# Kernel tuning notes

Hardware: AMD Instinct MI355X
Metric: run time of the kernel (lower is better)

The kernel has to match this reference:

```python
import jax, jax.numpy as jnp
import numpy as np

E = 1024
H = 16
DH = E // H  # projection_dim = 64


def setup_inputs() -> dict:
    key = jax.random.key(0)
    ks = jax.random.split(key, 6)
    B, S = 2, 2048
    s = 1.0 / np.sqrt(E)
    return {
        "features": jax.random.normal(ks[0], (B, S, E), jnp.float32),
        "mask": jnp.zeros((B, 1, 1, S), jnp.float32),
        "Wq": jax.random.normal(ks[1], (E, E), jnp.float32) * s,
        "bq": jnp.zeros((E,), jnp.float32),
        "Wk": jax.random.normal(ks[2], (E, E), jnp.float32) * s,
        "bk": jnp.zeros((E,), jnp.float32),
        "Wv": jax.random.normal(ks[3], (E, E), jnp.float32) * s,
        "bv": jnp.zeros((E,), jnp.float32),
        "Wo": jax.random.normal(ks[4], (E, E), jnp.float32) * s,
        "bo": jnp.zeros((E,), jnp.float32),
    }


def _split_heads(x, B):
    # [B,S,E] -> [B,H,S,DH]
    return x.reshape(B, -1, H, DH).transpose(0, 2, 1, 3)


def reference(features, mask, Wq, bq, Wk, bk, Wv, bv, Wo, bo):
    B, S, _ = features.shape
    q = _split_heads(features @ Wq + bq, B)  # [B,H,S,DH]
    k = _split_heads(features @ Wk + bk, B)
    v = _split_heads(features @ Wv + bv, B)
    logits = jnp.einsum("bhqd,bhkd->bhqk", q, k) / jnp.sqrt(jnp.float32(DH))
    logits = logits + mask * (-1e9)
    attn = jax.nn.softmax(logits, axis=-1)  # [B,H,S,S]
    ctx = jnp.einsum("bhqk,bhkd->bhqd", attn, v)
    ctx = ctx.transpose(0, 2, 1, 3).reshape(B, S, E)
    out = ctx @ Wo + bo
    return out, attn
```

## Files before the change

### kernel.cpp

```cpp
#include <hip/hip_runtime.h>
#include <hip/hip_bf16.h>

typedef __attribute__((ext_vector_type(8))) short bf16x8;
typedef __attribute__((ext_vector_type(4))) float f32x4;

#define B_ 2
#define S_ 2048
#define E_ 1024
#define H_ 16
#define DH_ 64

__global__ __launch_bounds__(256) void cast_bf16_kernel(const float* __restrict__ x,
                                                        __hip_bfloat16* __restrict__ y) {
  int i = blockIdx.x * 256 + threadIdx.x;
  float4 v = reinterpret_cast<const float4*>(x)[i];
  __hip_bfloat16 t[4] = {__float2bfloat16(v.x), __float2bfloat16(v.y),
                         __float2bfloat16(v.z), __float2bfloat16(v.w)};
  reinterpret_cast<uint2*>(y)[i] = *reinterpret_cast<uint2*>(t);
}

__global__ __launch_bounds__(256) void transpose_cast_kernel(const float* __restrict__ W,
                                                             __hip_bfloat16* __restrict__ Wt) {
  __shared__ float t[32][33];
  int bx = blockIdx.x * 32, by = blockIdx.y * 32;
  int tx = threadIdx.x & 31, ty = threadIdx.x >> 5;
  for (int r = 0; r < 32; r += 8)
    t[ty + r][tx] = W[(size_t)(by + ty + r) * E_ + bx + tx];
  __syncthreads();
  for (int r = 0; r < 32; r += 8)
    Wt[(size_t)(bx + ty + r) * E_ + by + tx] = __float2bfloat16(t[tx][ty + r]);
}

#define GT 64
#define GBK 32
__global__ __launch_bounds__(256) void gemm_bt_kernel(
    const __hip_bfloat16* __restrict__ A,
    const __hip_bfloat16* __restrict__ Bt,
    const float* __restrict__ bias_m,
    const float* __restrict__ bias_n,
    __hip_bfloat16* __restrict__ Cb,
    float* __restrict__ Cf,
    int M, int N, int K) {
  __shared__ __hip_bfloat16 As[GT][GBK + 8];
  __shared__ __hip_bfloat16 Bs[GT][GBK + 8];
  const int tid = threadIdx.x;
  const int lane = tid & 63;
  const int wave = tid >> 6;
  const int l15 = lane & 15, l4 = lane >> 4;
  const int m0 = blockIdx.y * GT;
  const int n0 = blockIdx.x * GT;
  const int wm = (wave & 1) * 32;
  const int wn = (wave >> 1) * 32;
  const int srow = tid >> 2;
  const int schunk = (tid & 3) * 8;
  f32x4 acc[2][2] = {};
  for (int k0 = 0; k0 < K; k0 += GBK) {
    __syncthreads();
    *reinterpret_cast<bf16x8*>(&As[srow][schunk]) =
        *reinterpret_cast<const bf16x8*>(&A[(size_t)(m0 + srow) * K + k0 + schunk]);
    *reinterpret_cast<bf16x8*>(&Bs[srow][schunk]) =
        *reinterpret_cast<const bf16x8*>(&Bt[(size_t)(n0 + srow) * K + k0 + schunk]);
    __syncthreads();
    bf16x8 af[2], bfr[2];
#pragma unroll
    for (int i = 0; i < 2; ++i)
      af[i] = *reinterpret_cast<const bf16x8*>(&As[wm + i * 16 + l15][l4 * 8]);
#pragma unroll
    for (int j = 0; j < 2; ++j)
      bfr[j] = *reinterpret_cast<const bf16x8*>(&Bs[wn + j * 16 + l15][l4 * 8]);
#pragma unroll
    for (int i = 0; i < 2; ++i)
#pragma unroll
      for (int j = 0; j < 2; ++j)
        acc[i][j] = __builtin_amdgcn_mfma_f32_16x16x32_bf16(af[i], bfr[j], acc[i][j], 0, 0, 0);
  }
#pragma unroll
  for (int i = 0; i < 2; ++i)
#pragma unroll
    for (int j = 0; j < 2; ++j)
#pragma unroll
      for (int r = 0; r < 4; ++r) {
        int row = m0 + wm + i * 16 + l4 * 4 + r;
        int col = n0 + wn + j * 16 + l15;
        float v = acc[i][j][r];
        if (bias_m) v += bias_m[row];
        if (bias_n) v += bias_n[col];
        if (Cf) Cf[(size_t)row * N + col] = v;
        else    Cb[(size_t)row * N + col] = __float2bfloat16(v);
      }
}

#define QBLK 64
#define KBLK 128
__global__ __launch_bounds__(256) void attn_kernel(
    const __hip_bfloat16* __restrict__ Qb,
    const __hip_bfloat16* __restrict__ Kb,
    const __hip_bfloat16* __restrict__ Vtb,
    const float* __restrict__ mask,
    float* __restrict__ attn_out,
    __hip_bfloat16* __restrict__ Ctxb) {
  __shared__ __hip_bfloat16 Qs[QBLK][DH_ + 8];
  __shared__ __hip_bfloat16 Ks[KBLK][DH_ + 8];
  __shared__ __hip_bfloat16 Vs[DH_][KBLK + 8];
  __shared__ __hip_bfloat16 Ps[QBLK][KBLK + 8];
  const int tid = threadIdx.x;
  const int lane = tid & 63;
  const int wave = tid >> 6;
  const int l15 = lane & 15, l4 = lane >> 4;
  const int bh = blockIdx.y;
  const int b = bh >> 4;
  const int h = bh & 15;
  const int q0 = blockIdx.x * QBLK;

  {
    int row = tid >> 3, c = (tid & 7) * 8;
#pragma unroll
    for (int p = 0; p < 2; ++p) {
      int r = row + p * 32;
      *reinterpret_cast<bf16x8*>(&Qs[r][c]) =
          *reinterpret_cast<const bf16x8*>(&Qb[(size_t)(b * S_ + q0 + r) * E_ + h * DH_ + c]);
    }
  }
  __syncthreads();
  bf16x8 qa0 = *reinterpret_cast<const bf16x8*>(&Qs[wave * 16 + l15][l4 * 8]);
  bf16x8 qa1 = *reinterpret_cast<const bf16x8*>(&Qs[wave * 16 + l15][32 + l4 * 8]);

  float mrow[4], srow[4];
#pragma unroll
  for (int r = 0; r < 4; ++r) { mrow[r] = -1e30f; srow[r] = 0.f; }

  for (int kt = 0; kt < S_ / KBLK; ++kt) {
    __syncthreads();
    { int row = tid >> 3, c = (tid & 7) * 8;
#pragma unroll
      for (int p = 0; p < 4; ++p) {
        int r = row + p * 32;
        *reinterpret_cast<bf16x8*>(&Ks[r][c]) =
            *reinterpret_cast<const bf16x8*>(&Kb[(size_t)(b * S_ + kt * KBLK + r) * E_ + h * DH_ + c]);
      }
    }
    __syncthreads();
    f32x4 sv[8];
#pragma unroll
    for (int j = 0; j < 8; ++j) {
      bf16x8 kb0 = *reinterpret_cast<const bf16x8*>(&Ks[j * 16 + l15][l4 * 8]);
      bf16x8 kb1 = *reinterpret_cast<const bf16x8*>(&Ks[j * 16 + l15][32 + l4 * 8]);
      f32x4 a = {};
      a = __builtin_amdgcn_mfma_f32_16x16x32_bf16(qa0, kb0, a, 0, 0, 0);
      a = __builtin_amdgcn_mfma_f32_16x16x32_bf16(qa1, kb1, a, 0, 0, 0);
      float mv = mask[b * S_ + kt * KBLK + j * 16 + l15] * -1e9f;
#pragma unroll
      for (int r = 0; r < 4; ++r) sv[j][r] = a[r] * 0.125f + mv;
    }
#pragma unroll
    for (int r = 0; r < 4; ++r) {
      float tmax = sv[0][r];
#pragma unroll
      for (int j = 1; j < 8; ++j) tmax = fmaxf(tmax, sv[j][r]);
      for (int m = 1; m < 16; m <<= 1) tmax = fmaxf(tmax, __shfl_xor(tmax, m, 64));
      float newm = fmaxf(mrow[r], tmax);
      float ls = 0.f;
#pragma unroll
      for (int j = 0; j < 8; ++j) ls += __expf(sv[j][r] - newm);
      for (int m = 1; m < 16; m <<= 1) ls += __shfl_xor(ls, m, 64);
      srow[r] = srow[r] * __expf(mrow[r] - newm) + ls;
      mrow[r] = newm;
    }
  }
  float inv_s[4];
#pragma unroll
  for (int r = 0; r < 4; ++r) inv_s[r] = 1.0f / srow[r];

  f32x4 ctx[4] = {};
  float* attn_base = attn_out + (size_t)bh * S_ * S_;
  for (int kt = 0; kt < S_ / KBLK; ++kt) {
    __syncthreads();
    { int row = tid >> 3, c = (tid & 7) * 8;
#pragma unroll
      for (int p = 0; p < 4; ++p) {
        int r = row + p * 32;
        *reinterpret_cast<bf16x8*>(&Ks[r][c]) =
            *reinterpret_cast<const bf16x8*>(&Kb[(size_t)(b * S_ + kt * KBLK + r) * E_ + h * DH_ + c]);
      }
    }
    { int d = tid >> 4, c = (tid & 15) * 8;
#pragma unroll
      for (int p = 0; p < 4; ++p) {
        int dd = d + p * 16;
        *reinterpret_cast<bf16x8*>(&Vs[dd][c]) =
            *reinterpret_cast<const bf16x8*>(&Vtb[(size_t)(h * DH_ + dd) * (B_ * S_) + b * S_ + kt * KBLK + c]);
      }
    }
    __syncthreads();
#pragma unroll
    for (int j = 0; j < 8; ++j) {
      bf16x8 kb0 = *reinterpret_cast<const bf16x8*>(&Ks[j * 16 + l15][l4 * 8]);
      bf16x8 kb1 = *reinterpret_cast<const bf16x8*>(&Ks[j * 16 + l15][32 + l4 * 8]);
      f32x4 a = {};
      a = __builtin_amdgcn_mfma_f32_16x16x32_bf16(qa0, kb0, a, 0, 0, 0);
      a = __builtin_amdgcn_mfma_f32_16x16x32_bf16(qa1, kb1, a, 0, 0, 0);
      float mv = mask[b * S_ + kt * KBLK + j * 16 + l15] * -1e9f;
#pragma unroll
      for (int r = 0; r < 4; ++r) {
        float p = __expf(a[r] * 0.125f + mv - mrow[r]) * inv_s[r];
        int row = wave * 16 + l4 * 4 + r;
        int col = j * 16 + l15;
        attn_base[(size_t)(q0 + row) * S_ + kt * KBLK + col] = p;
        Ps[row][col] = __float2bfloat16(p);
      }
    }
    __syncthreads();
#pragma unroll
    for (int kk = 0; kk < 4; ++kk) {
      bf16x8 pa = *reinterpret_cast<const bf16x8*>(&Ps[wave * 16 + l15][kk * 32 + l4 * 8]);
#pragma unroll
      for (int j2 = 0; j2 < 4; ++j2) {
        bf16x8 vb = *reinterpret_cast<const bf16x8*>(&Vs[j2 * 16 + l15][kk * 32 + l4 * 8]);
        ctx[j2] = __builtin_amdgcn_mfma_f32_16x16x32_bf16(pa, vb, ctx[j2], 0, 0, 0);
      }
    }
  }
#pragma unroll
  for (int j2 = 0; j2 < 4; ++j2)
#pragma unroll
    for (int r = 0; r < 4; ++r) {
      int row = wave * 16 + l4 * 4 + r;
      int col = j2 * 16 + l15;
      Ctxb[(size_t)(b * S_ + q0 + row) * E_ + h * DH_ + col] = __float2bfloat16(ctx[j2][r]);
    }
}

extern "C" void kernel_launch(void* const* d_in, const int* in_sizes, int n_in,
                              void* d_out, int out_size, void* d_ws, size_t ws_size,
                              hipStream_t stream) {
  const float* features = (const float*)d_in[0];
  const float* mask     = (const float*)d_in[1];
  const float* Wq       = (const float*)d_in[2];
  const float* bq       = (const float*)d_in[3];
  const float* Wk       = (const float*)d_in[4];
  const float* bk       = (const float*)d_in[5];
  const float* Wv       = (const float*)d_in[6];
  const float* bv       = (const float*)d_in[7];
  const float* Wo       = (const float*)d_in[8];
  const float* bo       = (const float*)d_in[9];
  float* out  = (float*)d_out;
  float* attn = out + (size_t)B_ * S_ * E_;

  char* ws = (char*)d_ws;
  __hip_bfloat16* Xbf  = (__hip_bfloat16*)(ws);
  __hip_bfloat16* WqT  = (__hip_bfloat16*)(ws + (8ull  << 20));
  __hip_bfloat16* WkT  = (__hip_bfloat16*)(ws + (10ull << 20));
  __hip_bfloat16* WvT  = (__hip_bfloat16*)(ws + (12ull << 20));
  __hip_bfloat16* WoT  = (__hip_bfloat16*)(ws + (14ull << 20));
  __hip_bfloat16* Qb   = (__hip_bfloat16*)(ws + (16ull << 20));
  __hip_bfloat16* Kb   = (__hip_bfloat16*)(ws + (24ull << 20));
  __hip_bfloat16* Vtb  = (__hip_bfloat16*)(ws + (32ull << 20));
  __hip_bfloat16* Ctxb = (__hip_bfloat16*)(ws + (40ull << 20));

  cast_bf16_kernel<<<(B_ * S_ * E_ / 4) / 256, 256, 0, stream>>>(features, Xbf);
  dim3 tg(E_ / 32, E_ / 32);
  transpose_cast_kernel<<<tg, 256, 0, stream>>>(Wq, WqT);
  transpose_cast_kernel<<<tg, 256, 0, stream>>>(Wk, WkT);
  transpose_cast_kernel<<<tg, 256, 0, stream>>>(Wv, WvT);
  transpose_cast_kernel<<<tg, 256, 0, stream>>>(Wo, WoT);

  gemm_bt_kernel<<<dim3(E_ / GT, B_ * S_ / GT), 256, 0, stream>>>(
      Xbf, WqT, nullptr, bq, Qb, nullptr, B_ * S_, E_, E_);
  gemm_bt_kernel<<<dim3(E_ / GT, B_ * S_ / GT), 256, 0, stream>>>(
      Xbf, WkT, nullptr, bk, Kb, nullptr, B_ * S_, E_, E_);
  gemm_bt_kernel<<<dim3(B_ * S_ / GT, E_ / GT), 256, 0, stream>>>(
      WvT, Xbf, bv, nullptr, Vtb, nullptr, E_, B_ * S_, E_);

  attn_kernel<<<dim3(S_ / QBLK, B_ * H_), 256, 0, stream>>>(Qb, Kb, Vtb, mask, attn, Ctxb);

  gemm_bt_kernel<<<dim3(E_ / GT, B_ * S_ / GT), 256, 0, stream>>>(
      Ctxb, WoT, nullptr, bo, nullptr, out, B_ * S_, E_, E_);
}
```

Measured before the change: 817.2 us.

## Enlarge GEMM tiles with direct LDS loads and drop shared staging in attention

The GEMM moves from 64x64 to 128x128 tiles with 4x4 MFMA accumulators per wave and loads global data straight into LDS through global_load_lds, which raises arithmetic intensity and cuts the register round trip. The attention kernel stops staging Q/K/V in shared memory and reads MFMA fragments directly from global memory. It keeps only a per-wave P buffer, so the block-wide barriers go away. The 64MB attention-probability output is now written with nontemporal stores to bypass cache pollution. The risks are fewer GEMM blocks (256 per launch) on a large CU count, uncoalesced global fragment reads for K and V, and an LDS layout without padding that may cause bank conflicts.

```diff
diff --git a/kernel.cpp b/kernel.cpp
--- a/kernel.cpp
+++ b/kernel.cpp
@@ -31,9 +31,16 @@
     Wt[(size_t)(bx + ty + r) * E_ + by + tx] = __float2bfloat16(t[tx][ty + r]);
 }
 
-#define GT 64
-#define GBK 32
-__global__ __launch_bounds__(256) void gemm_bt_kernel(
+__device__ __forceinline__ void load16_to_lds(const __hip_bfloat16* g, __hip_bfloat16* l) {
+  __builtin_amdgcn_global_load_lds(
+      (const __attribute__((address_space(1))) void*)g,
+      (__attribute__((address_space(3))) void*)l, 16, 0, 0);
+}
+
+#define BM 128
+#define BN 128
+#define BKK 32
+__global__ __launch_bounds__(256) void gemm128_kernel(
     const __hip_bfloat16* __restrict__ A,
     const __hip_bfloat16* __restrict__ Bt,
     const float* __restrict__ bias_m,
@@ -41,43 +48,45 @@
     __hip_bfloat16* __restrict__ Cb,
     float* __restrict__ Cf,
     int M, int N, int K) {
-  __shared__ __hip_bfloat16 As[GT][GBK + 8];
-  __shared__ __hip_bfloat16 Bs[GT][GBK + 8];
+  __shared__ __align__(16) __hip_bfloat16 As[BM][BKK];
+  __shared__ __align__(16) __hip_bfloat16 Bs[BN][BKK];
   const int tid = threadIdx.x;
   const int lane = tid & 63;
   const int wave = tid >> 6;
   const int l15 = lane & 15, l4 = lane >> 4;
-  const int m0 = blockIdx.y * GT;
-  const int n0 = blockIdx.x * GT;
-  const int wm = (wave & 1) * 32;
-  const int wn = (wave >> 1) * 32;
-  const int srow = tid >> 2;
-  const int schunk = (tid & 3) * 8;
-  f32x4 acc[2][2] = {};
-  for (int k0 = 0; k0 < K; k0 += GBK) {
+  const int m0 = blockIdx.y * BM;
+  const int n0 = blockIdx.x * BN;
+  const int wm = (wave & 1) * 64;
+  const int wn = (wave >> 1) * 64;
+  const int sr = lane >> 2;
+  const int sc = (lane & 3) * 8;
+  f32x4 acc[4][4] = {};
+  for (int k0 = 0; k0 < K; k0 += BKK) {
     __syncthreads();
-    *reinterpret_cast<bf16x8*>(&As[srow][schunk]) =
-        *reinterpret_cast<const bf16x8*>(&A[(size_t)(m0 + srow) * K + k0 + schunk]);
-    *reinterpret_cast<bf16x8*>(&Bs[srow][schunk]) =
-        *reinterpret_cast<const bf16x8*>(&Bt[(size_t)(n0 + srow) * K + k0 + schunk]);
+#pragma unroll
+    for (int p = 0; p < 2; ++p) {
+      int r0 = wave * 32 + p * 16;
+      load16_to_lds(&A[(size_t)(m0 + r0 + sr) * K + k0 + sc], &As[r0][0]);
+      load16_to_lds(&Bt[(size_t)(n0 + r0 + sr) * K + k0 + sc], &Bs[r0][0]);
+    }
     __syncthreads();
-    bf16x8 af[2], bfr[2];
-#pragma unroll
-    for (int i = 0; i < 2; ++i)
+    bf16x8 af[4], bfr[4];
+#pragma unroll
+    for (int i = 0; i < 4; ++i)
       af[i] = *reinterpret_cast<const bf16x8*>(&As[wm + i * 16 + l15][l4 * 8]);
 #pragma unroll
-    for (int j = 0; j < 2; ++j)
+    for (int j = 0; j < 4; ++j)
       bfr[j] = *reinterpret_cast<const bf16x8*>(&Bs[wn + j * 16 + l15][l4 * 8]);
 #pragma unroll
-    for (int i = 0; i < 2; ++i)
-#pragma unroll
-      for (int j = 0; j < 2; ++j)
+    for (int i = 0; i < 4; ++i)
+#pragma unroll
+      for (int j = 0; j < 4; ++j)
         acc[i][j] = __builtin_amdgcn_mfma_f32_16x16x32_bf16(af[i], bfr[j], acc[i][j], 0, 0, 0);
   }
 #pragma unroll
-  for (int i = 0; i < 2; ++i)
-#pragma unroll
-    for (int j = 0; j < 2; ++j)
+  for (int i = 0; i < 4; ++i)
+#pragma unroll
+    for (int j = 0; j < 4; ++j)
 #pragma unroll
       for (int r = 0; r < 4; ++r) {
         int row = m0 + wm + i * 16 + l4 * 4 + r;
@@ -99,10 +108,7 @@
     const float* __restrict__ mask,
     float* __restrict__ attn_out,
     __hip_bfloat16* __restrict__ Ctxb) {
-  __shared__ __hip_bfloat16 Qs[QBLK][DH_ + 8];
-  __shared__ __hip_bfloat16 Ks[KBLK][DH_ + 8];
-  __shared__ __hip_bfloat16 Vs[DH_][KBLK + 8];
-  __shared__ __hip_bfloat16 Ps[QBLK][KBLK + 8];
+  __shared__ __align__(16) __hip_bfloat16 Ps[4][16][KBLK + 8];
   const int tid = threadIdx.x;
   const int lane = tid & 63;
   const int wave = tid >> 6;
@@ -111,40 +117,24 @@
   const int b = bh >> 4;
   const int h = bh & 15;
   const int q0 = blockIdx.x * QBLK;
-
-  {
-    int row = tid >> 3, c = (tid & 7) * 8;
-#pragma unroll
-    for (int p = 0; p < 2; ++p) {
-      int r = row + p * 32;
-      *reinterpret_cast<bf16x8*>(&Qs[r][c]) =
-          *reinterpret_cast<const bf16x8*>(&Qb[(size_t)(b * S_ + q0 + r) * E_ + h * DH_ + c]);
-    }
-  }
-  __syncthreads();
-  bf16x8 qa0 = *reinterpret_cast<const bf16x8*>(&Qs[wave * 16 + l15][l4 * 8]);
-  bf16x8 qa1 = *reinterpret_cast<const bf16x8*>(&Qs[wave * 16 + l15][32 + l4 * 8]);
+  const size_t tokbase = (size_t)b * S_;
+
+  const __hip_bfloat16* qp = &Qb[(tokbase + q0 + wave * 16 + l15) * E_ + h * DH_ + l4 * 8];
+  bf16x8 qa0 = *reinterpret_cast<const bf16x8*>(qp);
+  bf16x8 qa1 = *reinterpret_cast<const bf16x8*>(qp + 32);
 
   float mrow[4], srow[4];
 #pragma unroll
   for (int r = 0; r < 4; ++r) { mrow[r] = -1e30f; srow[r] = 0.f; }
 
   for (int kt = 0; kt < S_ / KBLK; ++kt) {
-    __syncthreads();
-    { int row = tid >> 3, c = (tid & 7) * 8;
-#pragma unroll
-      for (int p = 0; p < 4; ++p) {
-        int r = row + p * 32;
-        *reinterpret_cast<bf16x8*>(&Ks[r][c]) =
-            *reinterpret_cast<const bf16x8*>(&Kb[(size_t)(b * S_ + kt * KBLK + r) * E_ + h * DH_ + c]);
-      }
-    }
-    __syncthreads();
     f32x4 sv[8];
 #pragma unroll
     for (int j = 0; j < 8; ++j) {
-      bf16x8 kb0 = *reinterpret_cast<const bf16x8*>(&Ks[j * 16 + l15][l4 * 8]);
-      bf16x8 kb1 = *reinterpret_cast<const bf16x8*>(&Ks[j * 16 + l15][32 + l4 * 8]);
+      const __hip_bfloat16* kp =
+          &Kb[(tokbase + kt * KBLK + j * 16 + l15) * E_ + h * DH_ + l4 * 8];
+      bf16x8 kb0 = *reinterpret_cast<const bf16x8*>(kp);
+      bf16x8 kb1 = *reinterpret_cast<const bf16x8*>(kp + 32);
       f32x4 a = {};
       a = __builtin_amdgcn_mfma_f32_16x16x32_bf16(qa0, kb0, a, 0, 0, 0);
       a = __builtin_amdgcn_mfma_f32_16x16x32_bf16(qa1, kb1, a, 0, 0, 0);
@@ -174,28 +164,12 @@
   f32x4 ctx[4] = {};
   float* attn_base = attn_out + (size_t)bh * S_ * S_;
   for (int kt = 0; kt < S_ / KBLK; ++kt) {
-    __syncthreads();
-    { int row = tid >> 3, c = (tid & 7) * 8;
-#pragma unroll
-      for (int p = 0; p < 4; ++p) {
-        int r = row + p * 32;
-        *reinterpret_cast<bf16x8*>(&Ks[r][c]) =
-            *reinterpret_cast<const bf16x8*>(&Kb[(size_t)(b * S_ + kt * KBLK + r) * E_ + h * DH_ + c]);
-      }
-    }
-    { int d = tid >> 4, c = (tid & 15) * 8;
-#pragma unroll
-      for (int p = 0; p < 4; ++p) {
-        int dd = d + p * 16;
-        *reinterpret_cast<bf16x8*>(&Vs[dd][c]) =
-            *reinterpret_cast<const bf16x8*>(&Vtb[(size_t)(h * DH_ + dd) * (B_ * S_) + b * S_ + kt * KBLK + c]);
-      }
-    }
-    __syncthreads();
 #pragma unroll
     for (int j = 0; j < 8; ++j) {
-      bf16x8 kb0 = *reinterpret_cast<const bf16x8*>(&Ks[j * 16 + l15][l4 * 8]);
-      bf16x8 kb1 = *reinterpret_cast<const bf16x8*>(&Ks[j * 16 + l15][32 + l4 * 8]);
+      const __hip_bfloat16* kp =
+          &Kb[(tokbase + kt * KBLK + j * 16 + l15) * E_ + h * DH_ + l4 * 8];
+      bf16x8 kb0 = *reinterpret_cast<const bf16x8*>(kp);
+      bf16x8 kb1 = *reinterpret_cast<const bf16x8*>(kp + 32);
       f32x4 a = {};
       a = __builtin_amdgcn_mfma_f32_16x16x32_bf16(qa0, kb0, a, 0, 0, 0);
       a = __builtin_amdgcn_mfma_f32_16x16x32_bf16(qa1, kb1, a, 0, 0, 0);
@@ -203,19 +177,22 @@
 #pragma unroll
       for (int r = 0; r < 4; ++r) {
         float p = __expf(a[r] * 0.125f + mv - mrow[r]) * inv_s[r];
-        int row = wave * 16 + l4 * 4 + r;
+        int row = l4 * 4 + r;
         int col = j * 16 + l15;
-        attn_base[(size_t)(q0 + row) * S_ + kt * KBLK + col] = p;
-        Ps[row][col] = __float2bfloat16(p);
+        __builtin_nontemporal_store(
+            p, &attn_base[(size_t)(q0 + wave * 16 + row) * S_ + kt * KBLK + col]);
+        Ps[wave][row][col] = __float2bfloat16(p);
       }
     }
-    __syncthreads();
 #pragma unroll
     for (int kk = 0; kk < 4; ++kk) {
-      bf16x8 pa = *reinterpret_cast<const bf16x8*>(&Ps[wave * 16 + l15][kk * 32 + l4 * 8]);
+      bf16x8 pa = *reinterpret_cast<const bf16x8*>(&Ps[wave][l15][kk * 32 + l4 * 8]);
 #pragma unroll
       for (int j2 = 0; j2 < 4; ++j2) {
-        bf16x8 vb = *reinterpret_cast<const bf16x8*>(&Vs[j2 * 16 + l15][kk * 32 + l4 * 8]);
+        const __hip_bfloat16* vp =
+            &Vtb[(size_t)(h * DH_ + j2 * 16 + l15) * (B_ * S_) +
+                 tokbase + kt * KBLK + kk * 32 + l4 * 8];
+        bf16x8 vb = *reinterpret_cast<const bf16x8*>(vp);
         ctx[j2] = __builtin_amdgcn_mfma_f32_16x16x32_bf16(pa, vb, ctx[j2], 0, 0, 0);
       }
     }
@@ -226,7 +203,7 @@
     for (int r = 0; r < 4; ++r) {
       int row = wave * 16 + l4 * 4 + r;
       int col = j2 * 16 + l15;
-      Ctxb[(size_t)(b * S_ + q0 + row) * E_ + h * DH_ + col] = __float2bfloat16(ctx[j2][r]);
+      Ctxb[(tokbase + q0 + row) * E_ + h * DH_ + col] = __float2bfloat16(ctx[j2][r]);
     }
 }
 
@@ -264,15 +241,15 @@
   transpose_cast_kernel<<<tg, 256, 0, stream>>>(Wv, WvT);
   transpose_cast_kernel<<<tg, 256, 0, stream>>>(Wo, WoT);
 
-  gemm_bt_kernel<<<dim3(E_ / GT, B_ * S_ / GT), 256, 0, stream>>>(
+  gemm128_kernel<<<dim3(E_ / BN, B_ * S_ / BM), 256, 0, stream>>>(
       Xbf, WqT, nullptr, bq, Qb, nullptr, B_ * S_, E_, E_);
-  gemm_bt_kernel<<<dim3(E_ / GT, B_ * S_ / GT), 256, 0, stream>>>(
+  gemm128_kernel<<<dim3(E_ / BN, B_ * S_ / BM), 256, 0, stream>>>(
       Xbf, WkT, nullptr, bk, Kb, nullptr, B_ * S_, E_, E_);
-  gemm_bt_kernel<<<dim3(B_ * S_ / GT, E_ / GT), 256, 0, stream>>>(
+  gemm128_kernel<<<dim3(B_ * S_ / BN, E_ / BM), 256, 0, stream>>>(
       WvT, Xbf, bv, nullptr, Vtb, nullptr, E_, B_ * S_, E_);
 
   attn_kernel<<<dim3(S_ / QBLK, B_ * H_), 256, 0, stream>>>(Qb, Kb, Vtb, mask, attn, Ctxb);
 
-  gemm_bt_kernel<<<dim3(E_ / GT, B_ * S_ / GT), 256, 0, stream>>>(
+  gemm128_kernel<<<dim3(E_ / BN, B_ * S_ / BM), 256, 0, stream>>>(
       Ctxb, WoT, nullptr, bo, nullptr, out, B_ * S_, E_, E_);
 }
```

Measured after the change: 1.006 ms. 1.23x slower.
